# Performance work log

Hardware: AMD Instinct MI355X
Metric: run time of the kernel (lower is better)

## Reference

```python
import jax, jax.numpy as jnp
import numpy as np
from jax import lax

N = 200000
CIN = 64
COUT = 128
K = 27  # 3^3 kernel offsets
EPS = 1e-5


def _make_rulebook(key, n, k):
    ki, km = jax.random.split(key)
    idx = jax.random.randint(ki, (k, n), 0, n, dtype=jnp.int32)
    keep = jax.random.uniform(km, (k, n)) < 0.5
    idx = jnp.where(keep, idx, -1)
    # center offset is always the voxel itself (submanifold conv)
    idx = idx.at[k // 2].set(jnp.arange(n, dtype=jnp.int32))
    return idx


def setup_inputs() -> dict:
    key = jax.random.key(0)
    ks = jax.random.split(key, 8)
    feats = jax.random.normal(ks[0], (N, CIN), dtype=jnp.float32)
    nbr1 = _make_rulebook(ks[1], N, K)
    nbr2 = _make_rulebook(ks[2], N, K)
    W1 = jax.random.normal(ks[3], (K, CIN, COUT), dtype=jnp.float32) * 0.05
    W2 = jax.random.normal(ks[4], (K, COUT, COUT), dtype=jnp.float32) * 0.05
    Wd = jax.random.normal(ks[5], (CIN, COUT), dtype=jnp.float32) * 0.05
    g1 = jnp.ones((COUT,), jnp.float32); b1 = jnp.zeros((COUT,), jnp.float32)
    g2 = jnp.ones((COUT,), jnp.float32); b2 = jnp.zeros((COUT,), jnp.float32)
    gd = jnp.ones((COUT,), jnp.float32); bd = jnp.zeros((COUT,), jnp.float32)
    return dict(feats=feats, nbr1=nbr1, nbr2=nbr2, W1=W1, W2=W2, Wd=Wd,
                g1=g1, b1=b1, g2=g2, b2=b2, gd=gd, bd=bd)


def sparse_conv(feats, W, nbr):
    """Rulebook sparse conv: gather neighbors per offset, GEMM, accumulate.
    feats: [N, Cin]; W: [K, Cin, Cout]; nbr: [K, N] int (-1 = missing)."""
    n = feats.shape[0]
    acc0 = jnp.zeros((n, W.shape[-1]), feats.dtype)

    def body(acc, xs):
        idx, Wk = xs  # [N], [Cin, Cout]
        valid = (idx >= 0).astype(feats.dtype)[:, None]
        g = feats[jnp.clip(idx, 0)] * valid  # masked gather [N, Cin]
        return acc + g @ Wk, None

    out, _ = lax.scan(body, acc0, (nbr, W))
    return out


def batchnorm(x, gamma, beta):
    mean = jnp.mean(x, axis=0)
    var = jnp.var(x, axis=0)
    return (x - mean) * lax.rsqrt(var + EPS) * gamma + beta


def reference(feats, nbr1, nbr2, W1, W2, Wd, g1, b1, g2, b2, gd, bd):
    h = sparse_conv(feats, W1, nbr1)
    h = jax.nn.relu(batchnorm(h, g1, b1))
    h = sparse_conv(h, W2, nbr2)
    h = batchnorm(h, g2, b2)
    skip = batchnorm(feats @ Wd, gd, bd)  # 1x1 conv downsample (Cin != Cout)
    return jax.nn.relu(h + skip)
```

## Files before the change

kernel.cpp:

```cpp
#include <hip/hip_runtime.h>
#include <stdint.h>

#define KOFF 27
#define CIN 64
#define COUT 128
#define EPS 1e-5f

using frag_ab = __attribute__((ext_vector_type(8))) short;
using frag_cd = __attribute__((ext_vector_type(4))) float;

__device__ __forceinline__ float bf2f(unsigned short u) {
  union { unsigned int i; float f; } x; x.i = ((unsigned int)u) << 16; return x.f;
}
__device__ __forceinline__ unsigned short f2bf(float f) {
  union { float f; unsigned int i; } x; x.f = f;
  unsigned int u = x.i;
  u += 0x7fffu + ((u >> 16) & 1u);
  return (unsigned short)(u >> 16);
}

__device__ __forceinline__ void gld16(const void* gptr, void* lptr) {
  __builtin_amdgcn_global_load_lds(
      (const __attribute__((address_space(1))) unsigned int*)gptr,
      (__attribute__((address_space(3))) unsigned int*)lptr, 16, 0, 0);
}

template <int CI, bool GATHER, bool OF32>
__global__ __launch_bounds__(256, 3) void conv_kernel(
    const unsigned short* __restrict__ X, const int* __restrict__ nbr,
    const unsigned short* __restrict__ Wt, void* __restrict__ Yv,
    const unsigned short* __restrict__ zpage, float* __restrict__ sums,
    int n, int koff) {
  constexpr int NC = CI / 32;
  __shared__ unsigned short Alds[3][128 * 32];

  const int tid = threadIdx.x;
  const int lane = tid & 63;
  const int wave = tid >> 6;
  const int row0 = blockIdx.x * 128;
  const int wrow = (wave >> 1) * 64;
  const int wcol = (wave & 1) * 64;
  const int m = lane & 15;
  const int q = lane >> 4;
  const int srow0 = wave * 16 + (lane >> 2);
  const int sl = lane & 3;

  frag_cd acc[4][4];
#pragma unroll
  for (int i = 0; i < 4; ++i)
#pragma unroll
    for (int j = 0; j < 4; ++j) acc[i][j] = (frag_cd){0.f, 0.f, 0.f, 0.f};

  frag_ab bA[4], bB[4];
  int idxc[2], idxn[2];

  auto load_idx = [&](int ko, int (&dst)[2]) {
#pragma unroll
    for (int i = 0; i < 2; ++i) {
      const int grow = row0 + srow0 + i * 64;
      int v = -1;
      if (grow < n) v = GATHER ? nbr[(size_t)ko * n + grow] : grow;
      dst[i] = v;
    }
  };
  auto stageA = [&](int buf, int ko, int kc, const int (&idx)[2]) {
#pragma unroll
    for (int i = 0; i < 2; ++i) {
      const int row = srow0 + i * 64;
      const int g = sl ^ ((row >> 1) & 3);
      const unsigned short* ga =
          (idx[i] >= 0) ? X + (size_t)idx[i] * CI + kc * 32 + g * 8 : zpage;
      gld16(ga, &Alds[buf][(i * 64 + wave * 16) * 32]);
    }
  };
  auto loadB = [&](frag_ab (&b)[4], int ko, int kc) {
    const unsigned short* base =
        Wt + (size_t)(ko * NC + kc) * 4096 + q * 1024 + m * 8;
#pragma unroll
    for (int j = 0; j < 4; ++j)
      b[j] = *(const frag_ab*)(base + (wcol + 16 * j) * 8);
  };
  auto do_mfma = [&](int buf, frag_ab (&b)[4]) {
    frag_ab a[4];
#pragma unroll
    for (int i = 0; i < 4; ++i) {
      const int row = wrow + 16 * i + m;
      a[i] = *(const frag_ab*)(&Alds[buf][row * 32 + (q ^ ((row >> 1) & 3)) * 8]);
    }
#pragma unroll
    for (int i = 0; i < 4; ++i)
#pragma unroll
      for (int j = 0; j < 4; ++j)
        acc[i][j] = __builtin_amdgcn_mfma_f32_16x16x32_bf16(a[i], b[j],
                                                            acc[i][j], 0, 0, 0);
  };

  const int T = koff * NC;
  load_idx(0, idxc);
  if (koff > 1) load_idx(1, idxn);
  stageA(0, 0, 0, idxc);
  stageA(1, 0, 1, idxc);
  loadB(bA, 0, 0);

  int bufc = 0;
  auto body = [&](int t, frag_ab (&bcur)[4], frag_ab (&bnxt)[4]) {
    asm volatile("s_waitcnt vmcnt(6)" ::: "memory");
    __builtin_amdgcn_s_barrier();
    const int s = t + 2;
    if (s < T && GATHER) {
      const int kos = s / NC;
      if ((s & (NC - 1)) == 0) {
        idxc[0] = idxn[0];
        idxc[1] = idxn[1];
        if (kos + 1 < koff) load_idx(kos + 1, idxn);
      }
    }
    const int u = t + 1;
    if (u < T) loadB(bnxt, u / NC, u & (NC - 1));
    if (s < T) {
      int bufs = bufc + 2; if (bufs >= 3) bufs -= 3;
      stageA(bufs, s / NC, s & (NC - 1), idxc);
    }
    do_mfma(bufc, bcur);
    if (++bufc == 3) bufc = 0;
  };

  for (int t = 0; t + 3 < T; t += 2) {
    body(t, bA, bB);
    body(t + 1, bB, bA);
  }
  body(T - 2, bA, bB);
  asm volatile("s_waitcnt vmcnt(0)" ::: "memory");
  __builtin_amdgcn_s_barrier();
  do_mfma(bufc, bB);

#pragma unroll
  for (int j = 0; j < 4; ++j) {
    float s = 0.f, qq = 0.f;
#pragma unroll
    for (int i = 0; i < 4; ++i)
#pragma unroll
      for (int r = 0; r < 4; ++r) {
        float v = acc[i][j][r];
        s += v; qq += v * v;
      }
    s += __shfl_xor(s, 16); s += __shfl_xor(s, 32);
    qq += __shfl_xor(qq, 16); qq += __shfl_xor(qq, 32);
    if (lane < 16) {
      const int col = wcol + 16 * j + lane;
      atomicAdd(&sums[col], s);
      atomicAdd(&sums[COUT + col], qq);
    }
  }

#pragma unroll
  for (int i = 0; i < 4; ++i) {
#pragma unroll
    for (int r = 0; r < 4; ++r) {
      const int grow = row0 + wrow + 16 * i + q * 4 + r;
      if (grow < n) {
#pragma unroll
        for (int j = 0; j < 4; ++j) {
          const int gcol = wcol + 16 * j + m;
          if (OF32)
            ((float*)Yv)[(size_t)grow * COUT + gcol] = acc[i][j][r];
          else
            ((unsigned short*)Yv)[(size_t)grow * COUT + gcol] = f2bf(acc[i][j][r]);
        }
      }
    }
  }
}

__global__ void convert_kernel(const float* __restrict__ src,
                               unsigned short* __restrict__ dst, int total8) {
  int gid = blockIdx.x * 256 + threadIdx.x;
  if (gid >= total8) return;
  const float* s = src + (size_t)gid * 8;
  float4 lo = *(const float4*)s;
  float4 hi = *(const float4*)(s + 4);
  uint4 r;
  r.x = (unsigned)f2bf(lo.x) | ((unsigned)f2bf(lo.y) << 16);
  r.y = (unsigned)f2bf(lo.z) | ((unsigned)f2bf(lo.w) << 16);
  r.z = (unsigned)f2bf(hi.x) | ((unsigned)f2bf(hi.y) << 16);
  r.w = (unsigned)f2bf(hi.z) | ((unsigned)f2bf(hi.w) << 16);
  *(uint4*)(dst + (size_t)gid * 8) = r;
}

__global__ void transpose_w(const float* __restrict__ src,
                            unsigned short* __restrict__ dst, int koff,
                            int ci) {
  int gid = blockIdx.x * blockDim.x + threadIdx.x;
  int total = koff * ci * 128;
  if (gid >= total) return;
  int e = gid & 7;
  int co = (gid >> 3) & 127;
  int qq = (gid >> 10) & 3;
  int slab = gid >> 12;
  int nc = ci >> 5;
  int ko = slab / nc;
  int kc = slab - ko * nc;
  int cin = kc * 32 + qq * 8 + e;
  dst[gid] = f2bf(src[((size_t)ko * ci + cin) * 128 + co]);
}

__global__ void finalize_kernel(const float* __restrict__ sums,
                                const float* __restrict__ gamma,
                                const float* __restrict__ beta,
                                float* __restrict__ scale,
                                float* __restrict__ shift, int n) {
  int c = threadIdx.x;
  float inv_n = 1.f / (float)n;
  float mean = sums[c] * inv_n;
  float var = sums[COUT + c] * inv_n - mean * mean;
  float sc = gamma[c] * rsqrtf(var + EPS);
  scale[c] = sc;
  shift[c] = beta[c] - mean * sc;
}

__global__ void norm_relu_kernel(unsigned short* __restrict__ x,
                                 const float* __restrict__ scale,
                                 const float* __restrict__ shift, int total8) {
  int gid = blockIdx.x * 256 + threadIdx.x;
  if (gid >= total8) return;
  size_t i = (size_t)gid * 8;
  int c0 = (int)(i & 127);
  uint4 v = *(const uint4*)(x + i);
  unsigned int w[4] = {v.x, v.y, v.z, v.w};
  unsigned int wo[4];
#pragma unroll
  for (int e = 0; e < 4; ++e) {
    int c = c0 + 2 * e;
    float f0 = bf2f((unsigned short)(w[e] & 0xffffu));
    float f1 = bf2f((unsigned short)(w[e] >> 16));
    f0 = fmaxf(f0 * scale[c] + shift[c], 0.f);
    f1 = fmaxf(f1 * scale[c + 1] + shift[c + 1], 0.f);
    wo[e] = (unsigned int)f2bf(f0) | ((unsigned int)f2bf(f1) << 16);
  }
  *(uint4*)(x + i) = make_uint4(wo[0], wo[1], wo[2], wo[3]);
}

__global__ void final_kernel(float* __restrict__ h2,
                             const unsigned short* __restrict__ s,
                             const float* __restrict__ scale2,
                             const float* __restrict__ shift2,
                             const float* __restrict__ scaled,
                             const float* __restrict__ shiftd, int total4) {
  int gid = blockIdx.x * 256 + threadIdx.x;
  if (gid >= total4) return;
  size_t i = (size_t)gid * 4;
  int c = (int)(i & 127);
  float4 a = *(const float4*)(h2 + i);
  uint2 sv = *(const uint2*)(s + i);
  float b0 = bf2f((unsigned short)(sv.x & 0xffffu));
  float b1 = bf2f((unsigned short)(sv.x >> 16));
  float b2 = bf2f((unsigned short)(sv.y & 0xffffu));
  float b3 = bf2f((unsigned short)(sv.y >> 16));
  float4 o;
  o.x = fmaxf(a.x * scale2[c] + shift2[c] + b0 * scaled[c] + shiftd[c], 0.f);
  o.y = fmaxf(a.y * scale2[c + 1] + shift2[c + 1] + b1 * scaled[c + 1] + shiftd[c + 1], 0.f);
  o.z = fmaxf(a.z * scale2[c + 2] + shift2[c + 2] + b2 * scaled[c + 2] + shiftd[c + 2], 0.f);
  o.w = fmaxf(a.w * scale2[c + 3] + shift2[c + 3] + b3 * scaled[c + 3] + shiftd[c + 3], 0.f);
  *(float4*)(h2 + i) = o;
}

extern "C" void kernel_launch(void* const* d_in, const int* in_sizes, int n_in,
                              void* d_out, int out_size, void* d_ws,
                              size_t ws_size, hipStream_t stream) {
  (void)n_in; (void)out_size; (void)ws_size;
  const float* feats = (const float*)d_in[0];
  const int* nbr1 = (const int*)d_in[1];
  const int* nbr2 = (const int*)d_in[2];
  const float* W1 = (const float*)d_in[3];
  const float* W2 = (const float*)d_in[4];
  const float* Wd = (const float*)d_in[5];
  const float* g1 = (const float*)d_in[6];
  const float* b1 = (const float*)d_in[7];
  const float* g2 = (const float*)d_in[8];
  const float* b2 = (const float*)d_in[9];
  const float* gd = (const float*)d_in[10];
  const float* bd = (const float*)d_in[11];

  const int n = in_sizes[0] / CIN;

  char* ws = (char*)d_ws;
  unsigned short* Wt1 = (unsigned short*)(ws);
  unsigned short* Wt2 = (unsigned short*)(ws + 442368);
  unsigned short* Wdt = (unsigned short*)(ws + 1327104);
  unsigned short* h1 = (unsigned short*)(ws + 1343488);
  unsigned short* sX = (unsigned short*)(ws + 52543488);
  float* sums1 = (float*)(ws + 103743488);
  float* sums2 = sums1 + 2 * COUT;
  float* sumsd = sums1 + 4 * COUT;
  float* scale1 = sums1 + 6 * COUT;
  float* shift1 = scale1 + COUT;
  float* scale2 = scale1 + 2 * COUT;
  float* shift2 = scale1 + 3 * COUT;
  float* scaled = scale1 + 4 * COUT;
  float* shiftd = scale1 + 5 * COUT;
  unsigned short* zpage = (unsigned short*)(ws + 103743488 + 8192);

  float* h2 = (float*)d_out;
  unsigned short* featsb = (unsigned short*)((char*)d_out + 76800000);

  hipMemsetAsync(sums1, 0, 8192 + 256, stream);

  transpose_w<<<(KOFF * CIN * COUT + 255) / 256, 256, 0, stream>>>(W1, Wt1, KOFF, CIN);
  transpose_w<<<(KOFF * COUT * COUT + 255) / 256, 256, 0, stream>>>(W2, Wt2, KOFF, COUT);
  transpose_w<<<(CIN * COUT + 255) / 256, 256, 0, stream>>>(Wd, Wdt, 1, CIN);

  const int f8 = n * CIN / 8;
  convert_kernel<<<(f8 + 255) / 256, 256, 0, stream>>>(feats, featsb, f8);

  const int mblocks = (n + 127) / 128;
  conv_kernel<CIN, true, false><<<mblocks, 256, 0, stream>>>(featsb, nbr1, Wt1, h1, zpage, sums1, n, KOFF);
  conv_kernel<CIN, false, false><<<mblocks, 256, 0, stream>>>(featsb, nullptr, Wdt, sX, zpage, sumsd, n, 1);

  finalize_kernel<<<1, COUT, 0, stream>>>(sums1, g1, b1, scale1, shift1, n);

  const int total8 = n * COUT / 8;
  norm_relu_kernel<<<(total8 + 255) / 256, 256, 0, stream>>>(h1, scale1, shift1, total8);

  conv_kernel<COUT, true, true><<<mblocks, 256, 0, stream>>>(h1, nbr2, Wt2, h2, zpage, sums2, n, KOFF);

  finalize_kernel<<<1, COUT, 0, stream>>>(sums2, g2, b2, scale2, shift2, n);
  finalize_kernel<<<1, COUT, 0, stream>>>(sumsd, gd, bd, scaled, shiftd, n);

  const int total4 = n * COUT / 4;
  final_kernel<<<(total4 + 255) / 256, 256, 0, stream>>>(h2, sX, scale2, shift2, scaled, shiftd, total4);
}
```

Measured before the change: 696.0 us.

## Fuse feature conversion into skip GEMM and fold BN finalize into consumers

The fp32-to-bf16 feature conversion is merged with the 1x1 skip convolution in a new kernel, which writes featsb and fills LDS directly, so the converted features are not re-read for the skip GEMM. The weight transposes and the zeroing of the stats buffers are combined into one prep kernel, replacing a memset and three launches. The separate finalize kernels are removed: each block of the normalize and final kernels recomputes scale and shift in shared memory. This cuts launch count and one pass over the features, at the cost of redundant per-block BN math and in-kernel loads of Wd that are neither cached nor coalesced.

```diff
diff --git a/kernel.cpp b/kernel.cpp
--- a/kernel.cpp
+++ b/kernel.cpp
@@ -172,27 +172,128 @@
   }
 }
 
-__global__ void convert_kernel(const float* __restrict__ src,
-                               unsigned short* __restrict__ dst, int total8) {
+__global__ __launch_bounds__(256, 2) void convskip_kernel(
+    const float* __restrict__ feats, const float* __restrict__ Wd,
+    unsigned short* __restrict__ featsb, unsigned short* __restrict__ sX,
+    float* __restrict__ sums, int n) {
+  __shared__ unsigned short Alds[2][128 * 32];
+  const int tid = threadIdx.x;
+  const int lane = tid & 63;
+  const int wave = tid >> 6;
+  const int row0 = blockIdx.x * 128;
+  const int wrow = (wave >> 1) * 64;
+  const int wcol = (wave & 1) * 64;
+  const int m = lane & 15;
+  const int q = lane >> 4;
+
+#pragma unroll
+  for (int c = 0; c < 4; ++c) {
+    int u = c * 256 + tid;
+    int kc = u >> 9;
+    int v = u & 511;
+    int row = v >> 2;
+    int s = v & 3;
+    int g = s ^ ((row >> 1) & 3);
+    int grow = row0 + row;
+    uint4 out = make_uint4(0u, 0u, 0u, 0u);
+    if (grow < n) {
+      const float* p = feats + (size_t)grow * 64 + kc * 32 + g * 8;
+      float4 lo = *(const float4*)p;
+      float4 hi = *(const float4*)(p + 4);
+      out.x = (unsigned)f2bf(lo.x) | ((unsigned)f2bf(lo.y) << 16);
+      out.y = (unsigned)f2bf(lo.z) | ((unsigned)f2bf(lo.w) << 16);
+      out.z = (unsigned)f2bf(hi.x) | ((unsigned)f2bf(hi.y) << 16);
+      out.w = (unsigned)f2bf(hi.z) | ((unsigned)f2bf(hi.w) << 16);
+      *(uint4*)(featsb + (size_t)grow * 64 + kc * 32 + g * 8) = out;
+    }
+    *(uint4*)(&Alds[kc][row * 32 + s * 8]) = out;
+  }
+  __syncthreads();
+
+  frag_cd acc[4][4];
+#pragma unroll
+  for (int i = 0; i < 4; ++i)
+#pragma unroll
+    for (int j = 0; j < 4; ++j) acc[i][j] = (frag_cd){0.f, 0.f, 0.f, 0.f};
+
+#pragma unroll
+  for (int kc = 0; kc < 2; ++kc) {
+    frag_ab b[4];
+#pragma unroll
+    for (int j = 0; j < 4; ++j) {
+      const int co = wcol + 16 * j + m;
+#pragma unroll
+      for (int e = 0; e < 8; ++e)
+        b[j][e] = (short)f2bf(Wd[(size_t)(kc * 32 + q * 8 + e) * 128 + co]);
+    }
+    frag_ab a[4];
+#pragma unroll
+    for (int i = 0; i < 4; ++i) {
+      const int row = wrow + 16 * i + m;
+      a[i] = *(const frag_ab*)(&Alds[kc][row * 32 + (q ^ ((row >> 1) & 3)) * 8]);
+    }
+#pragma unroll
+    for (int i = 0; i < 4; ++i)
+#pragma unroll
+      for (int j = 0; j < 4; ++j)
+        acc[i][j] = __builtin_amdgcn_mfma_f32_16x16x32_bf16(a[i], b[j],
+                                                            acc[i][j], 0, 0, 0);
+  }
+
+#pragma unroll
+  for (int j = 0; j < 4; ++j) {
+    float s = 0.f, qq = 0.f;
+#pragma unroll
+    for (int i = 0; i < 4; ++i)
+#pragma unroll
+      for (int r = 0; r < 4; ++r) {
+        float v = acc[i][j][r];
+        s += v; qq += v * v;
+      }
+    s += __shfl_xor(s, 16); s += __shfl_xor(s, 32);
+    qq += __shfl_xor(qq, 16); qq += __shfl_xor(qq, 32);
+    if (lane < 16) {
+      const int col = wcol + 16 * j + lane;
+      atomicAdd(&sums[col], s);
+      atomicAdd(&sums[COUT + col], qq);
+    }
+  }
+
+#pragma unroll
+  for (int i = 0; i < 4; ++i) {
+#pragma unroll
+    for (int r = 0; r < 4; ++r) {
+      const int grow = row0 + wrow + 16 * i + q * 4 + r;
+      if (grow < n) {
+#pragma unroll
+        for (int j = 0; j < 4; ++j)
+          sX[(size_t)grow * COUT + wcol + 16 * j + m] = f2bf(acc[i][j][r]);
+      }
+    }
+  }
+}
+
+__global__ void prep_kernel(const float* __restrict__ W1,
+                            const float* __restrict__ W2,
+                            unsigned short* __restrict__ Wt1,
+                            unsigned short* __restrict__ Wt2,
+                            float* __restrict__ zbase,
+                            float* __restrict__ zpage) {
+  const int NZ = 768 + 64;
+  const int NW1 = KOFF * CIN * 128;
+  const int NW2 = KOFF * COUT * 128;
   int gid = blockIdx.x * 256 + threadIdx.x;
-  if (gid >= total8) return;
-  const float* s = src + (size_t)gid * 8;
-  float4 lo = *(const float4*)s;
-  float4 hi = *(const float4*)(s + 4);
-  uint4 r;
-  r.x = (unsigned)f2bf(lo.x) | ((unsigned)f2bf(lo.y) << 16);
-  r.y = (unsigned)f2bf(lo.z) | ((unsigned)f2bf(lo.w) << 16);
-  r.z = (unsigned)f2bf(hi.x) | ((unsigned)f2bf(hi.y) << 16);
-  r.w = (unsigned)f2bf(hi.z) | ((unsigned)f2bf(hi.w) << 16);
-  *(uint4*)(dst + (size_t)gid * 8) = r;
-}
-
-__global__ void transpose_w(const float* __restrict__ src,
-                            unsigned short* __restrict__ dst, int koff,
-                            int ci) {
-  int gid = blockIdx.x * blockDim.x + threadIdx.x;
-  int total = koff * ci * 128;
-  if (gid >= total) return;
+  if (gid < NZ) {
+    if (gid < 768) zbase[gid] = 0.f; else zpage[gid - 768] = 0.f;
+    return;
+  }
+  gid -= NZ;
+  const float* src;
+  unsigned short* dst;
+  int ci;
+  if (gid < NW1) { src = W1; dst = Wt1; ci = CIN; }
+  else if (gid < NW1 + NW2) { gid -= NW1; src = W2; dst = Wt2; ci = COUT; }
+  else return;
   int e = gid & 7;
   int co = (gid >> 3) & 127;
   int qq = (gid >> 10) & 3;
@@ -204,24 +305,23 @@
   dst[gid] = f2bf(src[((size_t)ko * ci + cin) * 128 + co]);
 }
 
-__global__ void finalize_kernel(const float* __restrict__ sums,
-                                const float* __restrict__ gamma,
-                                const float* __restrict__ beta,
-                                float* __restrict__ scale,
-                                float* __restrict__ shift, int n) {
-  int c = threadIdx.x;
-  float inv_n = 1.f / (float)n;
-  float mean = sums[c] * inv_n;
-  float var = sums[COUT + c] * inv_n - mean * mean;
-  float sc = gamma[c] * rsqrtf(var + EPS);
-  scale[c] = sc;
-  shift[c] = beta[c] - mean * sc;
-}
-
 __global__ void norm_relu_kernel(unsigned short* __restrict__ x,
-                                 const float* __restrict__ scale,
-                                 const float* __restrict__ shift, int total8) {
-  int gid = blockIdx.x * 256 + threadIdx.x;
+                                 const float* __restrict__ sums,
+                                 const float* __restrict__ gamma,
+                                 const float* __restrict__ beta,
+                                 int n, int total8) {
+  __shared__ float sc[COUT], sh[COUT];
+  const int tid = threadIdx.x;
+  if (tid < COUT) {
+    float inv_n = 1.f / (float)n;
+    float mean = sums[tid] * inv_n;
+    float var = sums[COUT + tid] * inv_n - mean * mean;
+    float s = gamma[tid] * rsqrtf(var + EPS);
+    sc[tid] = s;
+    sh[tid] = beta[tid] - mean * s;
+  }
+  __syncthreads();
+  int gid = blockIdx.x * 256 + tid;
   if (gid >= total8) return;
   size_t i = (size_t)gid * 8;
   int c0 = (int)(i & 127);
@@ -233,8 +333,8 @@
     int c = c0 + 2 * e;
     float f0 = bf2f((unsigned short)(w[e] & 0xffffu));
     float f1 = bf2f((unsigned short)(w[e] >> 16));
-    f0 = fmaxf(f0 * scale[c] + shift[c], 0.f);
-    f1 = fmaxf(f1 * scale[c + 1] + shift[c + 1], 0.f);
+    f0 = fmaxf(f0 * sc[c] + sh[c], 0.f);
+    f1 = fmaxf(f1 * sc[c + 1] + sh[c + 1], 0.f);
     wo[e] = (unsigned int)f2bf(f0) | ((unsigned int)f2bf(f1) << 16);
   }
   *(uint4*)(x + i) = make_uint4(wo[0], wo[1], wo[2], wo[3]);
@@ -242,11 +342,30 @@
 
 __global__ void final_kernel(float* __restrict__ h2,
                              const unsigned short* __restrict__ s,
-                             const float* __restrict__ scale2,
-                             const float* __restrict__ shift2,
-                             const float* __restrict__ scaled,
-                             const float* __restrict__ shiftd, int total4) {
-  int gid = blockIdx.x * 256 + threadIdx.x;
+                             const float* __restrict__ sums2,
+                             const float* __restrict__ sumsd,
+                             const float* __restrict__ g2,
+                             const float* __restrict__ b2,
+                             const float* __restrict__ gd,
+                             const float* __restrict__ bd,
+                             int n, int total4) {
+  __shared__ float sc2[COUT], sh2[COUT], scd[COUT], shd[COUT];
+  const int tid = threadIdx.x;
+  if (tid < COUT) {
+    float inv_n = 1.f / (float)n;
+    float mean = sums2[tid] * inv_n;
+    float var = sums2[COUT + tid] * inv_n - mean * mean;
+    float sa = g2[tid] * rsqrtf(var + EPS);
+    sc2[tid] = sa;
+    sh2[tid] = b2[tid] - mean * sa;
+    mean = sumsd[tid] * inv_n;
+    var = sumsd[COUT + tid] * inv_n - mean * mean;
+    float sb = gd[tid] * rsqrtf(var + EPS);
+    scd[tid] = sb;
+    shd[tid] = bd[tid] - mean * sb;
+  }
+  __syncthreads();
+  int gid = blockIdx.x * 256 + tid;
   if (gid >= total4) return;
   size_t i = (size_t)gid * 4;
   int c = (int)(i & 127);
@@ -254,13 +373,13 @@
   uint2 sv = *(const uint2*)(s + i);
   float b0 = bf2f((unsigned short)(sv.x & 0xffffu));
   float b1 = bf2f((unsigned short)(sv.x >> 16));
-  float b2 = bf2f((unsigned short)(sv.y & 0xffffu));
+  float b2f = bf2f((unsigned short)(sv.y & 0xffffu));
   float b3 = bf2f((unsigned short)(sv.y >> 16));
   float4 o;
-  o.x = fmaxf(a.x * scale2[c] + shift2[c] + b0 * scaled[c] + shiftd[c], 0.f);
-  o.y = fmaxf(a.y * scale2[c + 1] + shift2[c + 1] + b1 * scaled[c + 1] + shiftd[c + 1], 0.f);
-  o.z = fmaxf(a.z * scale2[c + 2] + shift2[c + 2] + b2 * scaled[c + 2] + shiftd[c + 2], 0.f);
-  o.w = fmaxf(a.w * scale2[c + 3] + shift2[c + 3] + b3 * scaled[c + 3] + shiftd[c + 3], 0.f);
+  o.x = fmaxf(a.x * sc2[c] + sh2[c] + b0 * scd[c] + shd[c], 0.f);
+  o.y = fmaxf(a.y * sc2[c + 1] + sh2[c + 1] + b1 * scd[c + 1] + shd[c + 1], 0.f);
+  o.z = fmaxf(a.z * sc2[c + 2] + sh2[c + 2] + b2f * scd[c + 2] + shd[c + 2], 0.f);
+  o.w = fmaxf(a.w * sc2[c + 3] + sh2[c + 3] + b3 * scd[c + 3] + shd[c + 3], 0.f);
   *(float4*)(h2 + i) = o;
 }
 
@@ -286,46 +405,33 @@
   char* ws = (char*)d_ws;
   unsigned short* Wt1 = (unsigned short*)(ws);
   unsigned short* Wt2 = (unsigned short*)(ws + 442368);
-  unsigned short* Wdt = (unsigned short*)(ws + 1327104);
   unsigned short* h1 = (unsigned short*)(ws + 1343488);
   unsigned short* sX = (unsigned short*)(ws + 52543488);
   float* sums1 = (float*)(ws + 103743488);
   float* sums2 = sums1 + 2 * COUT;
   float* sumsd = sums1 + 4 * COUT;
-  float* scale1 = sums1 + 6 * COUT;
-  float* shift1 = scale1 + COUT;
-  float* scale2 = scale1 + 2 * COUT;
-  float* shift2 = scale1 + 3 * COUT;
-  float* scaled = scale1 + 4 * COUT;
-  float* shiftd = scale1 + 5 * COUT;
   unsigned short* zpage = (unsigned short*)(ws + 103743488 + 8192);
 
   float* h2 = (float*)d_out;
   unsigned short* featsb = (unsigned short*)((char*)d_out + 76800000);
 
-  hipMemsetAsync(sums1, 0, 8192 + 256, stream);
-
-  transpose_w<<<(KOFF * CIN * COUT + 255) / 256, 256, 0, stream>>>(W1, Wt1, KOFF, CIN);
-  transpose_w<<<(KOFF * COUT * COUT + 255) / 256, 256, 0, stream>>>(W2, Wt2, KOFF, COUT);
-  transpose_w<<<(CIN * COUT + 255) / 256, 256, 0, stream>>>(Wd, Wdt, 1, CIN);
-
-  const int f8 = n * CIN / 8;
-  convert_kernel<<<(f8 + 255) / 256, 256, 0, stream>>>(feats, featsb, f8);
+  const int prep_units = (768 + 64) + KOFF * CIN * 128 + KOFF * COUT * 128;
+  prep_kernel<<<(prep_units + 255) / 256, 256, 0, stream>>>(
+      W1, W2, Wt1, Wt2, sums1, (float*)zpage);
 
   const int mblocks = (n + 127) / 128;
-  conv_kernel<CIN, true, false><<<mblocks, 256, 0, stream>>>(featsb, nbr1, Wt1, h1, zpage, sums1, n, KOFF);
-  conv_kernel<CIN, false, false><<<mblocks, 256, 0, stream>>>(featsb, nullptr, Wdt, sX, zpage, sumsd, n, 1);
-
-  finalize_kernel<<<1, COUT, 0, stream>>>(sums1, g1, b1, scale1, shift1, n);
+  convskip_kernel<<<mblocks, 256, 0, stream>>>(feats, Wd, featsb, sX, sumsd, n);
+
+  conv_kernel<CIN, true, false><<<mblocks, 256, 0, stream>>>(
+      featsb, nbr1, Wt1, h1, zpage, sums1, n, KOFF);
 
   const int total8 = n * COUT / 8;
-  norm_relu_kernel<<<(total8 + 255) / 256, 256, 0, stream>>>(h1, scale1, shift1, total8);
-
-  conv_kernel<COUT, true, true><<<mblocks, 256, 0, stream>>>(h1, nbr2, Wt2, h2, zpage, sums2, n, KOFF);
-
-  finalize_kernel<<<1, COUT, 0, stream>>>(sums2, g2, b2, scale2, shift2, n);
-  finalize_kernel<<<1, COUT, 0, stream>>>(sumsd, gd, bd, scaled, shiftd, n);
+  norm_relu_kernel<<<(total8 + 255) / 256, 256, 0, stream>>>(h1, sums1, g1, b1, n, total8);
+
+  conv_kernel<COUT, true, true><<<mblocks, 256, 0, stream>>>(
+      h1, nbr2, Wt2, h2, zpage, sums2, n, KOFF);
 
   const int total4 = n * COUT / 4;
-  final_kernel<<<(total4 + 255) / 256, 256, 0, stream>>>(h2, sX, scale2, shift2, scaled, shiftd, total4);
-}
+  final_kernel<<<(total4 + 255) / 256, 256, 0, stream>>>(
+      h2, sX, sums2, sumsd, g2, b2, gd, bd, n, total4);
+}
```

Result: faster. 676.0 us (-2.9%).
